# Kernel tuning notes

Measured on AMD Instinct MI355X. Metric: run time of the kernel, lower is better.

## Reference

```python
import jax, jax.numpy as jnp
import numpy as np
from functools import partial

INPUT_SIZE = 24
HIDDEN = 64
NUM_LAYERS = 3
OUT_FEATURES = 4


def _lstm_layer(x, w_ih, w_hh, b_ih, b_hh):
    """Single LSTM layer, PyTorch gate order (i, f, g, o).
    x: [B, T, in] -> returns h sequence [B, T, H]."""
    B = x.shape[0]
    H = w_hh.shape[1]
    # Precompute input contribution for all timesteps: [B, T, 4H]
    gx = jnp.einsum('bti,gi->btg', x, w_ih) + b_ih + b_hh

    def step(carry, g_t):
        h, c = carry
        gates = g_t + h @ w_hh.T  # [B, 4H]
        i, f, g, o = jnp.split(gates, 4, axis=-1)
        i = jax.nn.sigmoid(i)
        f = jax.nn.sigmoid(f)
        g = jnp.tanh(g)
        o = jax.nn.sigmoid(o)
        c = f * c + i * g
        h = o * jnp.tanh(c)
        return (h, c), h

    h0 = jnp.zeros((B, H), dtype=x.dtype)
    c0 = jnp.zeros((B, H), dtype=x.dtype)
    (_, _), hs = jax.lax.scan(step, (h0, c0), jnp.swapaxes(gx, 0, 1))  # hs: [T, B, H]
    return jnp.swapaxes(hs, 0, 1)  # [B, T, H]


def setup_inputs() -> dict:
    key = jax.random.key(0)
    ks = jax.random.split(key, 16)
    B, T = 1024, 512
    inp = {"x": jax.random.normal(ks[0], (B, T, INPUT_SIZE), dtype=jnp.float32)}
    k = 1
    s = 1.0 / np.sqrt(HIDDEN)
    for layer in range(NUM_LAYERS):
        in_dim = INPUT_SIZE if layer == 0 else HIDDEN
        inp[f"w_ih_{layer}"] = jax.random.uniform(ks[k], (4 * HIDDEN, in_dim), minval=-s, maxval=s, dtype=jnp.float32); k += 1
        inp[f"w_hh_{layer}"] = jax.random.uniform(ks[k], (4 * HIDDEN, HIDDEN), minval=-s, maxval=s, dtype=jnp.float32); k += 1
        inp[f"b_ih_{layer}"] = jax.random.uniform(ks[k], (4 * HIDDEN,), minval=-s, maxval=s, dtype=jnp.float32); k += 1
        inp[f"b_hh_{layer}"] = jax.random.uniform(ks[k], (4 * HIDDEN,), minval=-s, maxval=s, dtype=jnp.float32); k += 1
    inp["w_lin"] = jax.random.uniform(ks[13], (OUT_FEATURES, HIDDEN), minval=-s, maxval=s, dtype=jnp.float32)
    inp["b_lin"] = jax.random.uniform(ks[14], (OUT_FEATURES,), minval=-s, maxval=s, dtype=jnp.float32)
    return inp


def reference(x, w_ih_0, w_hh_0, b_ih_0, b_hh_0,
              w_ih_1, w_hh_1, b_ih_1, b_hh_1,
              w_ih_2, w_hh_2, b_ih_2, b_hh_2,
              w_lin, b_lin):
    params = [(w_ih_0, w_hh_0, b_ih_0, b_hh_0),
              (w_ih_1, w_hh_1, b_ih_1, b_hh_1),
              (w_ih_2, w_hh_2, b_ih_2, b_hh_2)]
    h = x
    for (w_ih, w_hh, b_ih, b_hh) in params:  # fixed 3-layer stack
        h = _lstm_layer(h, w_ih, w_hh, b_ih, b_hh)
    last = h[:, -1]                      # [B, H]
    return last @ w_lin.T + b_lin        # [B, 4]
```

## Files before the change

kernel.cpp:

```cpp
#include <hip/hip_runtime.h>


typedef __attribute__((ext_vector_type(8))) _Float16 half8;
typedef __attribute__((ext_vector_type(4))) float floatx4;

static constexpr int T_STEPS = 512;

#define NL2E  (-1.4426950408889634f)
#define N2L2E (-2.8853900817779268f)

#define H_OFF0    0
#define H_OFF1    2048
#define H_OFF2    4096
#define FLAGS_OFF 6144
#define SM_BYTES  6208

__device__ __forceinline__ floatx4 mfma16(half8 a, half8 b, floatx4 c) {
    return __builtin_amdgcn_mfma_f32_16x16x32_f16(a, b, c, 0, 0, 0);
}

__device__ __forceinline__ half8 cvt8s(const float* src, float s) {
    float4 v0 = *(const float4*)(src);
    float4 v1 = *(const float4*)(src + 4);
    half8 h;
    h[0] = (_Float16)(v0.x * s); h[1] = (_Float16)(v0.y * s);
    h[2] = (_Float16)(v0.z * s); h[3] = (_Float16)(v0.w * s);
    h[4] = (_Float16)(v1.x * s); h[5] = (_Float16)(v1.y * s);
    h[6] = (_Float16)(v1.z * s); h[7] = (_Float16)(v1.w * s);
    return h;
}

__global__ __launch_bounds__(768, 3) void lstm3_async(
    const float* __restrict__ x,
    const float* __restrict__ w_ih0, const float* __restrict__ w_hh0,
    const float* __restrict__ b_ih0, const float* __restrict__ b_hh0,
    const float* __restrict__ w_ih1, const float* __restrict__ w_hh1,
    const float* __restrict__ b_ih1, const float* __restrict__ b_hh1,
    const float* __restrict__ w_ih2, const float* __restrict__ w_hh2,
    const float* __restrict__ b_ih2, const float* __restrict__ b_hh2,
    const float* __restrict__ w_lin, const float* __restrict__ b_lin,
    float* __restrict__ out)
{
    __shared__ __align__(16) char sm[SM_BYTES];
    int* dflag = (int*)(sm + FLAGS_OFF);

    const int tid  = threadIdx.x;
    const int lane = tid & 63;
    const int wave = tid >> 6;
    const int L    = wave >> 2;
    const int w    = wave & 3;
    const int l15  = lane & 15;
    const int l4   = lane >> 4;
    const int bat  = l15 >> 2;
    const int b0   = blockIdx.x * 4;
    const int u    = w * 16 + l15;

    for (int i = tid; i < SM_BYTES / 16; i += 768)
        *(floatx4*)(&sm[i * 16]) = floatx4{0.f, 0.f, 0.f, 0.f};

    const float* wi = (L == 0) ? w_ih0 : (L == 1 ? w_ih1 : w_ih2);
    const float* wh = (L == 0) ? w_hh0 : (L == 1 ? w_hh1 : w_hh2);
    const float* bi = (L == 0) ? b_ih0 : (L == 1 ? b_ih1 : b_ih2);
    const float* bh = (L == 0) ? b_hh0 : (L == 1 ? b_hh1 : b_hh2);
    const int HB = (L == 0) ? H_OFF0 : (L == 1 ? H_OFF1 : H_OFF2);
    const int PB = (L == 1) ? H_OFF0 : H_OFF1;

    half8 wf[4][4];
#pragma unroll
    for (int tt = 0; tt < 4; ++tt) {
        const int g = tt * 64 + u;
        const float sc = (tt == 2) ? N2L2E : NL2E;
        if (L == 0) {
            half8 z;
#pragma unroll
            for (int j = 0; j < 8; ++j) z[j] = (_Float16)0.f;
            wf[tt][0] = (l4 < 3) ? cvt8s(w_ih0 + g * 24 + l4 * 8, sc) : z;
            wf[tt][1] = cvt8s(w_hh0 + g * 64 + l4 * 8, sc);
            wf[tt][2] = cvt8s(w_hh0 + g * 64 + 32 + l4 * 8, sc);
            wf[tt][3] = z;
        } else {
            wf[tt][0] = cvt8s(wi + g * 64 + l4 * 8, sc);
            wf[tt][1] = cvt8s(wi + g * 64 + 32 + l4 * 8, sc);
            wf[tt][2] = cvt8s(wh + g * 64 + l4 * 8, sc);
            wf[tt][3] = cvt8s(wh + g * 64 + 32 + l4 * 8, sc);
        }
    }
    floatx4 bv[4];
#pragma unroll
    for (int tt = 0; tt < 4; ++tt) {
        const float sc = (tt == 2) ? N2L2E : NL2E;
        float b = sc * (bi[tt * 64 + u] + bh[tt * 64 + u]);
        bv[tt][0] = b; bv[tt][1] = b; bv[tt][2] = b; bv[tt][3] = b;
    }

    const int swzR = (bat & 1) << 5;
    int rb0 = 0, rb1 = 0, rb2 = 0, rb3 = 0;
    if (L == 0) {
        rb1 = H_OFF0 + ((bat * 128 + 0  + l4 * 16) ^ swzR);
        rb2 = H_OFF0 + ((bat * 128 + 64 + l4 * 16) ^ swzR);
    } else {
        rb0 = PB + ((bat * 128 + 0  + l4 * 16) ^ swzR);
        rb1 = PB + ((bat * 128 + 64 + l4 * 16) ^ swzR);
        rb2 = HB + ((bat * 128 + 0  + l4 * 16) ^ swzR);
        rb3 = HB + ((bat * 128 + 64 + l4 * 16) ^ swzR);
    }
    const int wb = HB + ((l4 * 128 + u * 2) ^ ((l4 & 1) << 5));

    float4 xA0{0,0,0,0}, xA1{0,0,0,0}, xB0{0,0,0,0}, xB1{0,0,0,0};
    const bool xv = (L == 0) && (l4 < 3);
    const float* xpe = nullptr;
    const float* xpo = nullptr;
    if (xv) {
        const float* xb_ = x + (long)(b0 + bat) * T_STEPS * 24 + l4 * 8;
        xA0 = *(const float4*)(xb_);      xA1 = *(const float4*)(xb_ + 4);
        xB0 = *(const float4*)(xb_ + 24); xB1 = *(const float4*)(xb_ + 28);
        xpe = xb_ + 48;
        xpo = xb_ + 72;
    }

    float cst = 0.0f;
    __syncthreads();

    auto step = [&](int t, int slot, int slotm1) __attribute__((always_inline)) {
        {
            const int TgA = (((t - 1) >> 2) + 1) * 4;
            volatile int* fA = dflag + L * 4 + slotm1;
            while (*fA < TgA) __builtin_amdgcn_s_sleep(1);
            if (L >= 1) {
                const int TgB = ((t >> 2) + 1) * 4;
                volatile int* fB = dflag + (L - 1) * 4 + slot;
                while (*fB < TgB) __builtin_amdgcn_s_sleep(1);
            }
            if (L <= 1) {
                const int TgC = (((t - 4) >> 2) + 1) * 4;
                volatile int* fC = dflag + (L + 1) * 4 + slot;
                while (*fC < TgC) __builtin_amdgcn_s_sleep(1);
            }
        }
        asm volatile("" ::: "memory");

        const int ro = slot * 512;
        const int rp = slotm1 * 512;

        floatx4 acc[4];
        __builtin_amdgcn_s_setprio(1);
        if (L == 0) {
            const float4 v0 = (slot & 1) ? xB0 : xA0;
            const float4 v1 = (slot & 1) ? xB1 : xA1;
            half8 aX;
            aX[0] = (_Float16)v0.x; aX[1] = (_Float16)v0.y;
            aX[2] = (_Float16)v0.z; aX[3] = (_Float16)v0.w;
            aX[4] = (_Float16)v1.x; aX[5] = (_Float16)v1.y;
            aX[6] = (_Float16)v1.z; aX[7] = (_Float16)v1.w;
            half8 a1 = *(const half8*)(&sm[rb1 + rp]);
            half8 a2 = *(const half8*)(&sm[rb2 + rp]);
#pragma unroll
            for (int tt = 0; tt < 4; ++tt) {
                acc[tt] = mfma16(aX, wf[tt][0], bv[tt]);
                acc[tt] = mfma16(a1, wf[tt][1], acc[tt]);
                acc[tt] = mfma16(a2, wf[tt][2], acc[tt]);
            }
            if (xv && t + 2 < T_STEPS) {
                if (slot & 1) {
                    xB0 = *(const float4*)(xpo); xB1 = *(const float4*)(xpo + 4);
                    xpo += 48;
                } else {
                    xA0 = *(const float4*)(xpe); xA1 = *(const float4*)(xpe + 4);
                    xpe += 48;
                }
            }
        } else {
            half8 a0 = *(const half8*)(&sm[rb0 + ro]);
            half8 a1 = *(const half8*)(&sm[rb1 + ro]);
            half8 a2 = *(const half8*)(&sm[rb2 + rp]);
            half8 a3 = *(const half8*)(&sm[rb3 + rp]);
#pragma unroll
            for (int tt = 0; tt < 4; ++tt) {
                acc[tt] = mfma16(a0, wf[tt][0], bv[tt]);
                acc[tt] = mfma16(a1, wf[tt][1], acc[tt]);
                acc[tt] = mfma16(a2, wf[tt][2], acc[tt]);
                acc[tt] = mfma16(a3, wf[tt][3], acc[tt]);
            }
        }
        __builtin_amdgcn_s_setprio(0);

        float ei = __builtin_amdgcn_exp2f(__builtin_amdgcn_fmed3f(acc[0][0], -30.f, 30.f));
        float ef = __builtin_amdgcn_exp2f(__builtin_amdgcn_fmed3f(acc[1][0], -30.f, 30.f));
        float eg = __builtin_amdgcn_exp2f(__builtin_amdgcn_fmed3f(acc[2][0], -30.f, 30.f));
        float eo = __builtin_amdgcn_exp2f(__builtin_amdgcn_fmed3f(acc[3][0], -30.f, 30.f));
        float A1 = 1.f + ei, B1 = 1.f + ef, C1 = 1.f + eg, D1 = 1.f + eo;
        float p = A1 * B1, q = C1 * D1;
        float r = __builtin_amdgcn_rcpf(p * q);
        float ip = r * q, iq = r * p;
        float ig = ip * B1;
        float fg = ip * A1;
        float sg = iq * D1;
        float og = iq * C1;
        float gg = fmaf(2.f, sg, -1.f);
        cst = fmaf(fg, cst, ig * gg);
        float et = __builtin_amdgcn_exp2f(cst * N2L2E);
        float th = fmaf(2.f, __builtin_amdgcn_rcpf(1.f + et), -1.f);
        float hv = og * th;
        *(_Float16*)(&sm[wb + ro]) = (_Float16)hv;

        asm volatile("s_waitcnt lgkmcnt(0)" ::: "memory");
        if (lane == 0) atomicAdd(dflag + L * 4 + slot, 1);
    };

    for (int tb = 0; tb < T_STEPS; tb += 4) {
        step(tb + 0, 0, 3);
        step(tb + 1, 1, 0);
        step(tb + 2, 2, 1);
        step(tb + 3, 3, 2);
    }

    __syncthreads();

    if (tid < 16) {
        const int bb = tid >> 2, o = tid & 3;
        float accum = b_lin[o];
#pragma unroll
        for (int k = 0; k < 64; ++k) {
            const int off = H_OFF2 + 3 * 512 + ((bb * 128 + k * 2) ^ ((bb & 1) << 5));
            accum = fmaf((float)*(const _Float16*)(&sm[off]), w_lin[o * 64 + k], accum);
        }
        out[(b0 + bb) * 4 + o] = accum;
    }
}

extern "C" void kernel_launch(void* const* d_in, const int* in_sizes, int n_in,
                              void* d_out, int out_size, void* d_ws, size_t ws_size,
                              hipStream_t stream) {
    const float* x     = (const float*)d_in[0];
    const float* w_ih0 = (const float*)d_in[1];
    const float* w_hh0 = (const float*)d_in[2];
    const float* b_ih0 = (const float*)d_in[3];
    const float* b_hh0 = (const float*)d_in[4];
    const float* w_ih1 = (const float*)d_in[5];
    const float* w_hh1 = (const float*)d_in[6];
    const float* b_ih1 = (const float*)d_in[7];
    const float* b_hh1 = (const float*)d_in[8];
    const float* w_ih2 = (const float*)d_in[9];
    const float* w_hh2 = (const float*)d_in[10];
    const float* b_ih2 = (const float*)d_in[11];
    const float* b_hh2 = (const float*)d_in[12];
    const float* w_lin = (const float*)d_in[13];
    const float* b_lin = (const float*)d_in[14];

    lstm3_async<<<dim3(256), dim3(768), 0, stream>>>(
        x, w_ih0, w_hh0, b_ih0, b_hh0,
        w_ih1, w_hh1, b_ih1, b_hh1,
        w_ih2, w_hh2, b_ih2, b_hh2,
        w_lin, b_lin, (float*)d_out);
}
```

Before: 336.7 us.

## Deepen LDS ring to 8 slots with per-wave step flags and split MFMA chains

Doubles the shared-memory hidden-state ring from 4 to 8 slots, so the lower layer may run up to 8 steps ahead of the one above. Per-slot atomic counters become per-wave flags holding the last finished step, and each step checks a prefetched int4 snapshot before falling back to polling. The MFMA accumulation is split into two independent chains to shorten the dependency latency, and the combined-reciprocal sigmoid trick is replaced by four separate rcp calls without clamping. The cost is more LDS use, extra flag reads per step, and possible overflow since exp2 inputs are no longer clamped.

```diff
diff --git a/kernel.cpp b/kernel.cpp
--- a/kernel.cpp
+++ b/kernel.cpp
@@ -10,10 +10,10 @@
 #define N2L2E (-2.8853900817779268f)
 
 #define H_OFF0    0
-#define H_OFF1    2048
-#define H_OFF2    4096
-#define FLAGS_OFF 6144
-#define SM_BYTES  6208
+#define H_OFF1    4096
+#define H_OFF2    8192
+#define FLAGS_OFF 12288
+#define SM_BYTES  12352
 
 __device__ __forceinline__ floatx4 mfma16(half8 a, half8 b, floatx4 c) {
     return __builtin_amdgcn_mfma_f32_16x16x32_f16(a, b, c, 0, 0, 0);
@@ -30,7 +30,7 @@
     return h;
 }
 
-__global__ __launch_bounds__(768, 3) void lstm3_async(
+__global__ __launch_bounds__(768, 3) void lstm3_ring(
     const float* __restrict__ x,
     const float* __restrict__ w_ih0, const float* __restrict__ w_hh0,
     const float* __restrict__ b_ih0, const float* __restrict__ b_hh0,
@@ -92,6 +92,7 @@
         float b = sc * (bi[tt * 64 + u] + bh[tt * 64 + u]);
         bv[tt][0] = b; bv[tt][1] = b; bv[tt][2] = b; bv[tt][3] = b;
     }
+    const floatx4 Z4 = floatx4{0.f, 0.f, 0.f, 0.f};
 
     const int swzR = (bat & 1) << 5;
     int rb0 = 0, rb1 = 0, rb2 = 0, rb3 = 0;
@@ -106,6 +107,11 @@
     }
     const int wb = HB + ((l4 * 128 + u * 2) ^ ((l4 & 1) << 5));
 
+    const int* fp_own = dflag + L * 4;
+    const int* fp_up  = (L >= 1) ? (dflag + (L - 1) * 4) : fp_own;
+    const int* fp_dn  = (L <= 1) ? (dflag + (L + 1) * 4) : fp_own;
+    int4 pf_own, pf_up, pf_dn;
+
     float4 xA0{0,0,0,0}, xA1{0,0,0,0}, xB0{0,0,0,0}, xB1{0,0,0,0};
     const bool xv = (L == 0) && (l4 < 3);
     const float* xpe = nullptr;
@@ -121,47 +127,53 @@
     float cst = 0.0f;
     __syncthreads();
 
-    auto step = [&](int t, int slot, int slotm1) __attribute__((always_inline)) {
-        {
-            const int TgA = (((t - 1) >> 2) + 1) * 4;
-            volatile int* fA = dflag + L * 4 + slotm1;
-            while (*fA < TgA) __builtin_amdgcn_s_sleep(1);
-            if (L >= 1) {
-                const int TgB = ((t >> 2) + 1) * 4;
-                volatile int* fB = dflag + (L - 1) * 4 + slot;
-                while (*fB < TgB) __builtin_amdgcn_s_sleep(1);
-            }
-            if (L <= 1) {
-                const int TgC = (((t - 4) >> 2) + 1) * 4;
-                volatile int* fC = dflag + (L + 1) * 4 + slot;
-                while (*fC < TgC) __builtin_amdgcn_s_sleep(1);
-            }
-        }
+    pf_own = *(const int4*)fp_own;
+    pf_up  = *(const int4*)fp_up;
+    pf_dn  = *(const int4*)fp_dn;
+
+    auto ok4 = [](int4 v, int tgt) -> bool {
+        return (v.x >= tgt) & (v.y >= tgt) & (v.z >= tgt) & (v.w >= tgt);
+    };
+    auto poll = [](const int* p, int tgt) {
+        for (;;) {
+            int a = ((const volatile int*)p)[0];
+            int b = ((const volatile int*)p)[1];
+            int c = ((const volatile int*)p)[2];
+            int d = ((const volatile int*)p)[3];
+            if (a >= tgt && b >= tgt && c >= tgt && d >= tgt) return;
+            __builtin_amdgcn_s_sleep(1);
+        }
+    };
+
+    auto step = [&](int t, int so, int sp) __attribute__((always_inline)) {
+        if (!ok4(pf_own, t))              poll(fp_own, t);
+        if (L >= 1 && !ok4(pf_up, t + 1)) poll(fp_up, t + 1);
+        if (L <= 1 && !ok4(pf_dn, t - 7)) poll(fp_dn, t - 7);
         asm volatile("" ::: "memory");
 
-        const int ro = slot * 512;
-        const int rp = slotm1 * 512;
-
-        floatx4 acc[4];
+        float pre0, pre1, pre2, pre3;
         __builtin_amdgcn_s_setprio(1);
         if (L == 0) {
-            const float4 v0 = (slot & 1) ? xB0 : xA0;
-            const float4 v1 = (slot & 1) ? xB1 : xA1;
+            const float4 v0 = (t & 1) ? xB0 : xA0;
+            const float4 v1 = (t & 1) ? xB1 : xA1;
             half8 aX;
             aX[0] = (_Float16)v0.x; aX[1] = (_Float16)v0.y;
             aX[2] = (_Float16)v0.z; aX[3] = (_Float16)v0.w;
             aX[4] = (_Float16)v1.x; aX[5] = (_Float16)v1.y;
             aX[6] = (_Float16)v1.z; aX[7] = (_Float16)v1.w;
-            half8 a1 = *(const half8*)(&sm[rb1 + rp]);
-            half8 a2 = *(const half8*)(&sm[rb2 + rp]);
+            half8 a1 = *(const half8*)(&sm[rb1 + sp]);
+            half8 a2 = *(const half8*)(&sm[rb2 + sp]);
 #pragma unroll
             for (int tt = 0; tt < 4; ++tt) {
-                acc[tt] = mfma16(aX, wf[tt][0], bv[tt]);
-                acc[tt] = mfma16(a1, wf[tt][1], acc[tt]);
-                acc[tt] = mfma16(a2, wf[tt][2], acc[tt]);
+                floatx4 accA = mfma16(aX, wf[tt][0], bv[tt]);
+                floatx4 accB = mfma16(a1, wf[tt][1], Z4);
+                accB = mfma16(a2, wf[tt][2], accB);
+                float p = accA[0] + accB[0];
+                if (tt == 0) pre0 = p; else if (tt == 1) pre1 = p;
+                else if (tt == 2) pre2 = p; else pre3 = p;
             }
             if (xv && t + 2 < T_STEPS) {
-                if (slot & 1) {
+                if (t & 1) {
                     xB0 = *(const float4*)(xpo); xB1 = *(const float4*)(xpo + 4);
                     xpo += 48;
                 } else {
@@ -170,48 +182,50 @@
                 }
             }
         } else {
-            half8 a0 = *(const half8*)(&sm[rb0 + ro]);
-            half8 a1 = *(const half8*)(&sm[rb1 + ro]);
-            half8 a2 = *(const half8*)(&sm[rb2 + rp]);
-            half8 a3 = *(const half8*)(&sm[rb3 + rp]);
+            half8 a0 = *(const half8*)(&sm[rb0 + so]);
+            half8 a1 = *(const half8*)(&sm[rb1 + so]);
+            half8 a2 = *(const half8*)(&sm[rb2 + sp]);
+            half8 a3 = *(const half8*)(&sm[rb3 + sp]);
 #pragma unroll
             for (int tt = 0; tt < 4; ++tt) {
-                acc[tt] = mfma16(a0, wf[tt][0], bv[tt]);
-                acc[tt] = mfma16(a1, wf[tt][1], acc[tt]);
-                acc[tt] = mfma16(a2, wf[tt][2], acc[tt]);
-                acc[tt] = mfma16(a3, wf[tt][3], acc[tt]);
+                floatx4 accA = mfma16(a0, wf[tt][0], bv[tt]);
+                floatx4 accB = mfma16(a2, wf[tt][2], Z4);
+                accA = mfma16(a1, wf[tt][1], accA);
+                accB = mfma16(a3, wf[tt][3], accB);
+                float p = accA[0] + accB[0];
+                if (tt == 0) pre0 = p; else if (tt == 1) pre1 = p;
+                else if (tt == 2) pre2 = p; else pre3 = p;
             }
         }
         __builtin_amdgcn_s_setprio(0);
 
-        float ei = __builtin_amdgcn_exp2f(__builtin_amdgcn_fmed3f(acc[0][0], -30.f, 30.f));
-        float ef = __builtin_amdgcn_exp2f(__builtin_amdgcn_fmed3f(acc[1][0], -30.f, 30.f));
-        float eg = __builtin_amdgcn_exp2f(__builtin_amdgcn_fmed3f(acc[2][0], -30.f, 30.f));
-        float eo = __builtin_amdgcn_exp2f(__builtin_amdgcn_fmed3f(acc[3][0], -30.f, 30.f));
-        float A1 = 1.f + ei, B1 = 1.f + ef, C1 = 1.f + eg, D1 = 1.f + eo;
-        float p = A1 * B1, q = C1 * D1;
-        float r = __builtin_amdgcn_rcpf(p * q);
-        float ip = r * q, iq = r * p;
-        float ig = ip * B1;
-        float fg = ip * A1;
-        float sg = iq * D1;
-        float og = iq * C1;
+        float ei = __builtin_amdgcn_exp2f(pre0);
+        float ef = __builtin_amdgcn_exp2f(pre1);
+        float eg = __builtin_amdgcn_exp2f(pre2);
+        float eo = __builtin_amdgcn_exp2f(pre3);
+        float ig = __builtin_amdgcn_rcpf(1.f + ei);
+        float fg = __builtin_amdgcn_rcpf(1.f + ef);
+        float sg = __builtin_amdgcn_rcpf(1.f + eg);
+        float og = __builtin_amdgcn_rcpf(1.f + eo);
         float gg = fmaf(2.f, sg, -1.f);
         cst = fmaf(fg, cst, ig * gg);
         float et = __builtin_amdgcn_exp2f(cst * N2L2E);
         float th = fmaf(2.f, __builtin_amdgcn_rcpf(1.f + et), -1.f);
         float hv = og * th;
-        *(_Float16*)(&sm[wb + ro]) = (_Float16)hv;
+        *(_Float16*)(&sm[wb + so]) = (_Float16)hv;
 
         asm volatile("s_waitcnt lgkmcnt(0)" ::: "memory");
-        if (lane == 0) atomicAdd(dflag + L * 4 + slot, 1);
+        if (lane == 0) ((volatile int*)dflag)[L * 4 + w] = t + 1;
+
+        pf_own = *(const int4*)fp_own;
+        if (L >= 1) pf_up = *(const int4*)fp_up;
+        if (L <= 1) pf_dn = *(const int4*)fp_dn;
     };
 
-    for (int tb = 0; tb < T_STEPS; tb += 4) {
-        step(tb + 0, 0, 3);
-        step(tb + 1, 1, 0);
-        step(tb + 2, 2, 1);
-        step(tb + 3, 3, 2);
+    for (int tb = 0; tb < T_STEPS; tb += 8) {
+#pragma unroll
+        for (int k = 0; k < 8; ++k)
+            step(tb + k, k * 512, ((k + 7) & 7) * 512);
     }
 
     __syncthreads();
@@ -221,7 +235,7 @@
         float accum = b_lin[o];
 #pragma unroll
         for (int k = 0; k < 64; ++k) {
-            const int off = H_OFF2 + 3 * 512 + ((bb * 128 + k * 2) ^ ((bb & 1) << 5));
+            const int off = H_OFF2 + 7 * 512 + ((bb * 128 + k * 2) ^ ((bb & 1) << 5));
             accum = fmaf((float)*(const _Float16*)(&sm[off]), w_lin[o * 64 + k], accum);
         }
         out[(b0 + bb) * 4 + o] = accum;
@@ -247,7 +261,7 @@
     const float* w_lin = (const float*)d_in[13];
     const float* b_lin = (const float*)d_in[14];
 
-    lstm3_async<<<dim3(256), dim3(768), 0, stream>>>(
+    lstm3_ring<<<dim3(256), dim3(768), 0, stream>>>(
         x, w_ih0, w_hh0, b_ih0, b_hh0,
         w_ih1, w_hh1, b_ih1, b_hh1,
         w_ih2, w_hh2, b_ih2, b_hh2,
```

New measurement: 482.3 us. 43.2% more time.
